# Optimization experiments

Measured on AMD Instinct MI355X. Metric: run time of the kernel, lower is better.

Reference implementation:

```python
import jax, jax.numpy as jnp
import numpy as np

EOS_IDX = 0  # CHARACTER_LIST.index(Config.EOS) stand-in


def _lstm_cell(x, h, c, W_ih, W_hh, b_ih, b_hh):
    # torch.nn.LSTMCell math; gate order i, f, g, o
    gates = x @ W_ih.T + b_ih + h @ W_hh.T + b_hh  # [B, 4H]
    i, f, g, o = jnp.split(gates, 4, axis=1)
    i = jax.nn.sigmoid(i)
    f = jax.nn.sigmoid(f)
    g = jnp.tanh(g)
    o = jax.nn.sigmoid(o)
    c_new = f * c + i * g
    h_new = o * jnp.tanh(c_new)
    return h_new, c_new


def setup_inputs() -> dict:
    key = jax.random.key(0)
    ks = jax.random.split(key, 13)
    B, T, V, E, H = 512, 256, 1000, 256, 512
    s = 0.05
    return {
        "listener_output": jax.random.normal(ks[0], (B, 128), jnp.float32),
        "ground_truth": jax.random.randint(ks[1], (B, T), 0, V, jnp.int64),
        "emb": jax.random.normal(ks[2], (V, E), jnp.float32) * s,
        "W_ih0": jax.random.normal(ks[3], (4 * H, E), jnp.float32) * s,
        "W_hh0": jax.random.normal(ks[4], (4 * H, H), jnp.float32) * s,
        "b_ih0": jax.random.normal(ks[5], (4 * H,), jnp.float32) * s,
        "b_hh0": jax.random.normal(ks[6], (4 * H,), jnp.float32) * s,
        "W_ih1": jax.random.normal(ks[7], (4 * H, E), jnp.float32) * s,
        "W_hh1": jax.random.normal(ks[8], (4 * H, H), jnp.float32) * s,
        "b_ih1": jax.random.normal(ks[9], (4 * H,), jnp.float32) * s,
        "b_hh1": jax.random.normal(ks[10], (4 * H,), jnp.float32) * s,
        "W_out": jax.random.normal(ks[11], (V, H), jnp.float32) * s,
        "b_out": jax.random.normal(ks[12], (V,), jnp.float32) * s,
    }


def reference(listener_output, ground_truth, emb, W_ih0, W_hh0, b_ih0, b_hh0,
              W_ih1, W_hh1, b_ih1, b_hh1, W_out, b_out):
    B = listener_output.shape[0]
    T = ground_truth.shape[1]
    H = W_hh0.shape[1]
    # Teacher forcing (ratio=1.0): input char at step 0 is EOS, then ground_truth[:, i-1]
    first = jnp.full((B, 1), EOS_IDX, dtype=ground_truth.dtype)
    chars = jnp.concatenate([first, ground_truth[:, :-1]], axis=1)  # [B, T]
    embeds = emb[chars]                                             # [B, T, E]
    xs = jnp.swapaxes(embeds, 0, 1)                                 # [T, B, E]

    h0 = jnp.zeros((B, H), embeds.dtype)
    c0 = jnp.zeros((B, H), embeds.dtype)
    h1 = jnp.zeros((B, H), embeds.dtype)
    c1 = jnp.zeros((B, H), embeds.dtype)

    def step(carry, x_t):
        h0, c0, h1, c1 = carry
        # Faithful to source: BOTH cells receive the embedding as input
        h0, c0 = _lstm_cell(x_t, h0, c0, W_ih0, W_hh0, b_ih0, b_hh0)
        h1, c1 = _lstm_cell(x_t, h1, c1, W_ih1, W_hh1, b_ih1, b_hh1)
        logits = h1 @ W_out.T + b_out                # [B, V]
        out = jax.nn.log_softmax(logits, axis=1)
        return (h0, c0, h1, c1), out

    _, outs = jax.lax.scan(step, (h0, c0, h1, c1), xs)  # [T, B, V]
    return jnp.swapaxes(outs, 0, 1)                     # [B, T, V]
```

## Files before the change

### kernel.cpp

```cpp
#include <hip/hip_runtime.h>
#include <hip/hip_bf16.h>

#define B_  512
#define T_  256
#define E_  256
#define H_  512
#define V_  1000
#define CH  16

typedef __attribute__((ext_vector_type(8))) short short8;
typedef __attribute__((ext_vector_type(4))) float f32x4;
typedef __hip_bfloat16 bf16;

#define MFMA16(a, b, c) __builtin_amdgcn_mfma_f32_16x16x32_bf16((a), (b), (c), 0, 0, 0)

__global__ void f32_to_bf16_kernel(const float* __restrict__ src,
                                   bf16* __restrict__ dst, int n8) {
  int i = blockIdx.x * blockDim.x + threadIdx.x;
  if (i >= n8) return;
  const float4* s4 = (const float4*)src;
  float4 a = s4[2 * i], b = s4[2 * i + 1];
  bf16 tmp[8] = {__float2bfloat16(a.x), __float2bfloat16(a.y),
                 __float2bfloat16(a.z), __float2bfloat16(a.w),
                 __float2bfloat16(b.x), __float2bfloat16(b.y),
                 __float2bfloat16(b.z), __float2bfloat16(b.w)};
  *(int4*)(dst + 8 * i) = *(const int4*)tmp;
}

__global__ __launch_bounds__(256) void embproj_kernel(
    const bf16* __restrict__ emb, const bf16* __restrict__ Wih,
    const float* __restrict__ b_ih, const float* __restrict__ b_hh,
    float* __restrict__ embProjB)
{
  __shared__ short As[64][40];
  __shared__ short Bs[64][40];
  const int tid  = threadIdx.x;
  const int wave = tid >> 6, lane = tid & 63;
  const int q = lane >> 4, col = lane & 15;
  const int m0 = blockIdx.x * 64;
  const int n0 = blockIdx.y * 64;
  const int sr  = tid >> 2, skc = (tid & 3) * 8;
  const int mr  = wave * 16 + col;
  const int ko  = q * 8;
  int arow = m0 + sr; if (arow > V_ - 1) arow = V_ - 1;

  f32x4 acc0 = {0.f,0.f,0.f,0.f}, acc1 = acc0, acc2 = acc0, acc3 = acc0;
  for (int k0 = 0; k0 < E_; k0 += 32) {
    *(int4*)&As[sr][skc] = *(const int4*)((const short*)emb + (size_t)arow * E_ + k0 + skc);
    *(int4*)&Bs[sr][skc] = *(const int4*)((const short*)Wih + (size_t)(n0 + sr) * E_ + k0 + skc);
    __syncthreads();
    short8 a  = *(const short8*)&As[mr][ko];
    short8 b0 = *(const short8*)&Bs[ 0 + col][ko];
    short8 b1 = *(const short8*)&Bs[16 + col][ko];
    short8 b2 = *(const short8*)&Bs[32 + col][ko];
    short8 b3 = *(const short8*)&Bs[48 + col][ko];
    acc0 = MFMA16(a, b0, acc0);
    acc1 = MFMA16(a, b1, acc1);
    acc2 = MFMA16(a, b2, acc2);
    acc3 = MFMA16(a, b3, acc3);
    __syncthreads();
  }
#pragma unroll
  for (int r = 0; r < 4; r++) {
    int m = m0 + wave * 16 + q * 4 + r;
    if (m < V_) {
      float* dst = embProjB + (size_t)m * 2048;
      int n = n0 + col;
      dst[n +  0] = acc0[r] + b_ih[n +  0] + b_hh[n +  0];
      dst[n + 16] = acc1[r] + b_ih[n + 16] + b_hh[n + 16];
      dst[n + 32] = acc2[r] + b_ih[n + 32] + b_hh[n + 32];
      dst[n + 48] = acc3[r] + b_ih[n + 48] + b_hh[n + 48];
    }
  }
}

__global__ __launch_bounds__(256) void recur_kernel(
    const int* __restrict__ gt,
    const bf16* __restrict__ Whh,
    const float* __restrict__ embProjB,
    const bf16* __restrict__ hprev0,
    bf16* __restrict__ h1buf,
    float* __restrict__ c_state,
    int* __restrict__ flags,
    int t0)
{
  __shared__ short Wl[64][520];
  __shared__ int chars[64];

  const int tid  = threadIdx.x;
  const int wave = tid >> 6, lane = tid & 63;
  const int q = lane >> 4, col = lane & 15;
  const int bid = blockIdx.x;
  const int mb = bid & 7, jb = bid >> 3;
  const int m0 = mb * 64, j0 = jb * 16;
  const int chunkv = (t0 >> 4) + 1;

  for (int cch = tid; cch < 64 * 64; cch += 256) {
    int r = cch >> 6, kc = (cch & 63) * 8;
    int gr = (r >> 4) * H_ + j0 + (r & 15);
    *(int4*)&Wl[r][kc] = *(const int4*)((const short*)Whh + (size_t)gr * H_ + kc);
  }

  const int mrow = m0 + wave * 16 + q * 4;
  const int arow = m0 + wave * 16 + col;

  float creg[4];
#pragma unroll
  for (int r = 0; r < 4; r++)
    creg[r] = c_state[(size_t)(mrow + r) * H_ + j0 + col];

  for (int s = 0; s < CH; s++) {
    const int t = t0 + s;
    if (tid < 64) chars[tid] = (t == 0) ? 0 : gt[(m0 + tid) * T_ + (t - 1)];
    if (s > 0 && tid < 32) {
      int* fl = flags + (((s - 1) * 8 + mb) << 5) + tid;
      while (__hip_atomic_load(fl, __ATOMIC_ACQUIRE, __HIP_MEMORY_SCOPE_AGENT) != chunkv) {}
    }
    __syncthreads();

    const bf16* hp = (s == 0) ? hprev0 : (h1buf + (size_t)(s - 1) * B_ * H_);

    float ex[4][4];
#pragma unroll
    for (int r = 0; r < 4; r++) {
      const float* ep = embProjB + (size_t)chars[wave * 16 + q * 4 + r] * 2048 + j0 + col;
#pragma unroll
      for (int g = 0; g < 4; g++) ex[g][r] = ep[g * H_];
    }

    f32x4 acc[4];
#pragma unroll
    for (int g = 0; g < 4; g++) acc[g] = (f32x4){0.f, 0.f, 0.f, 0.f};

    const short* abase = (const short*)hp + (size_t)arow * H_;
#pragma unroll
    for (int k0 = 0; k0 < H_; k0 += 32) {
      short8 a  = *(const short8*)(abase + k0 + q * 8);
      short8 b0 = *(const short8*)&Wl[ 0 + col][k0 + q * 8];
      short8 b1 = *(const short8*)&Wl[16 + col][k0 + q * 8];
      short8 b2 = *(const short8*)&Wl[32 + col][k0 + q * 8];
      short8 b3 = *(const short8*)&Wl[48 + col][k0 + q * 8];
      acc[0] = MFMA16(a, b0, acc[0]);
      acc[1] = MFMA16(a, b1, acc[1]);
      acc[2] = MFMA16(a, b2, acc[2]);
      acc[3] = MFMA16(a, b3, acc[3]);
    }

    bf16* ho = h1buf + (size_t)s * B_ * H_;
#pragma unroll
    for (int r = 0; r < 4; r++) {
      float iv = 1.f / (1.f + __expf(-(acc[0][r] + ex[0][r])));
      float fv = 1.f / (1.f + __expf(-(acc[1][r] + ex[1][r])));
      float gv = tanhf(acc[2][r] + ex[2][r]);
      float ov = 1.f / (1.f + __expf(-(acc[3][r] + ex[3][r])));
      float cN = fv * creg[r] + iv * gv;
      creg[r] = cN;
      ho[(size_t)(mrow + r) * H_ + j0 + col] = __float2bfloat16(ov * tanhf(cN));
    }

    __syncthreads();
    if (tid == 0)
      __hip_atomic_store(flags + ((s * 8 + mb) << 5) + jb, chunkv,
                         __ATOMIC_RELEASE, __HIP_MEMORY_SCOPE_AGENT);
  }

#pragma unroll
  for (int r = 0; r < 4; r++)
    c_state[(size_t)(mrow + r) * H_ + j0 + col] = creg[r];
}

__global__ __launch_bounds__(256) void out_proj_kernel(
    const bf16* __restrict__ h1buf,
    const bf16* __restrict__ Wout,
    const float* __restrict__ bout,
    float* __restrict__ out,
    int t0)
{
  __shared__ short Hs[32][520];
  __shared__ float red[4][32];
  __shared__ float rowM[32];
  __shared__ float rowS[32];

  const int tid  = threadIdx.x;
  const int wave = tid >> 6, lane = tid & 63;
  const int q = lane >> 4, col = lane & 15;
  const int s  = blockIdx.x >> 4;
  const int b0 = (blockIdx.x & 15) * 32;

  const short* hrow = (const short*)h1buf + ((size_t)s * B_ + b0) * H_;
  for (int c = tid; c < 2048; c += 256) {
    int r = c >> 6, kc = (c & 63) << 3;
    *(int4*)&Hs[r][kc] = *(const int4*)&hrow[r * H_ + kc];
  }
  __syncthreads();

  f32x4 acc[2][16];
#pragma unroll
  for (int mt = 0; mt < 2; mt++)
#pragma unroll
    for (int u = 0; u < 16; u++) acc[mt][u] = (f32x4){0.f, 0.f, 0.f, 0.f};

  const short* WS = (const short*)Wout;
  for (int k0 = 0; k0 < H_; k0 += 32) {
    short8 a0 = *(const short8*)&Hs[col][k0 + q * 8];
    short8 a1 = *(const short8*)&Hs[16 + col][k0 + q * 8];
#pragma unroll
    for (int u = 0; u < 16; u++) {
      int nt = wave + 4 * u;
      if (nt < 63) {
        int v = nt * 16 + col;
        int vc = v < V_ ? v : (V_ - 1);
        short8 bfr = *(const short8*)&WS[(size_t)vc * H_ + k0 + q * 8];
        acc[0][u] = MFMA16(a0, bfr, acc[0][u]);
        acc[1][u] = MFMA16(a1, bfr, acc[1][u]);
      }
    }
  }

  float bo[16];
  bool  val[16];
#pragma unroll
  for (int u = 0; u < 16; u++) {
    int nt = wave + 4 * u;
    int v = nt * 16 + col;
    val[u] = (nt < 63) && (v < V_);
    bo[u] = val[u] ? bout[v] : 0.f;
  }

  float mymax[2][4];
#pragma unroll
  for (int mt = 0; mt < 2; mt++)
#pragma unroll
    for (int r = 0; r < 4; r++) mymax[mt][r] = -1e30f;
#pragma unroll
  for (int mt = 0; mt < 2; mt++)
#pragma unroll
    for (int u = 0; u < 16; u++)
      if (val[u]) {
#pragma unroll
        for (int r = 0; r < 4; r++)
          mymax[mt][r] = fmaxf(mymax[mt][r], acc[mt][u][r] + bo[u]);
      }
#pragma unroll
  for (int d = 1; d < 16; d <<= 1)
#pragma unroll
    for (int mt = 0; mt < 2; mt++)
#pragma unroll
      for (int r = 0; r < 4; r++)
        mymax[mt][r] = fmaxf(mymax[mt][r], __shfl_xor(mymax[mt][r], d, 64));
  if (col == 0)
#pragma unroll
    for (int mt = 0; mt < 2; mt++)
#pragma unroll
      for (int r = 0; r < 4; r++)
        red[wave][mt * 16 + q * 4 + r] = mymax[mt][r];
  __syncthreads();
  if (tid < 32)
    rowM[tid] = fmaxf(fmaxf(red[0][tid], red[1][tid]),
                      fmaxf(red[2][tid], red[3][tid]));
  __syncthreads();

  float mysum[2][4] = {{0.f,0.f,0.f,0.f},{0.f,0.f,0.f,0.f}};
#pragma unroll
  for (int mt = 0; mt < 2; mt++)
#pragma unroll
    for (int r = 0; r < 4; r++) {
      float rm = rowM[mt * 16 + q * 4 + r];
#pragma unroll
      for (int u = 0; u < 16; u++)
        if (val[u]) mysum[mt][r] += __expf(acc[mt][u][r] + bo[u] - rm);
    }
#pragma unroll
  for (int d = 1; d < 16; d <<= 1)
#pragma unroll
    for (int mt = 0; mt < 2; mt++)
#pragma unroll
      for (int r = 0; r < 4; r++)
        mysum[mt][r] += __shfl_xor(mysum[mt][r], d, 64);
  if (col == 0)
#pragma unroll
    for (int mt = 0; mt < 2; mt++)
#pragma unroll
      for (int r = 0; r < 4; r++)
        red[wave][mt * 16 + q * 4 + r] = mysum[mt][r];
  __syncthreads();
  if (tid < 32)
    rowS[tid] = __logf(red[0][tid] + red[1][tid] + red[2][tid] + red[3][tid]);
  __syncthreads();

#pragma unroll
  for (int mt = 0; mt < 2; mt++)
#pragma unroll
    for (int r = 0; r < 4; r++) {
      int m = mt * 16 + q * 4 + r;
      float corr = rowM[m] + rowS[m];
      size_t base = ((size_t)(b0 + m) * T_ + (t0 + s)) * V_;
#pragma unroll
      for (int u = 0; u < 16; u++)
        if (val[u]) {
          int v = (wave + 4 * u) * 16 + col;
          out[base + v] = acc[mt][u][r] + bo[u] - corr;
        }
    }
}

extern "C" void kernel_launch(void* const* d_in, const int* in_sizes, int n_in,
                              void* d_out, int out_size, void* d_ws, size_t ws_size,
                              hipStream_t stream) {
  (void)in_sizes; (void)n_in; (void)out_size; (void)ws_size;
  const int*   gt     = (const int*)d_in[1];
  const float* emb_f  = (const float*)d_in[2];
  const float* Wih_f  = (const float*)d_in[7];
  const float* Whh_f  = (const float*)d_in[8];
  const float* b_ih1  = (const float*)d_in[9];
  const float* b_hh1  = (const float*)d_in[10];
  const float* Wout_f = (const float*)d_in[11];
  const float* bout   = (const float*)d_in[12];
  float* out = (float*)d_out;

  char* ws = (char*)d_ws;
  float* c_state = (float*)ws;
  bf16*  hinit   = (bf16*)(ws + 1048576);
  bf16*  h1buf   = (bf16*)(ws + 1572864);
  bf16*  emb_bf  = (bf16*)(ws + 9961472);
  bf16*  Wih_bf  = (bf16*)(ws + 10473472);
  bf16*  Whh_bf  = (bf16*)(ws + 11522048);
  bf16*  Wout_bf = (bf16*)(ws + 13619200);
  float* embP    = (float*)(ws + 14643200);
  int*   flags   = (int*)(ws + 22835200);

  hipMemsetAsync(d_ws, 0, 1572864, stream);
  hipMemsetAsync(flags, 0, 16384, stream);

  f32_to_bf16_kernel<<<(V_ * E_ / 8 + 255) / 256, 256, 0, stream>>>(emb_f, emb_bf, V_ * E_ / 8);
  f32_to_bf16_kernel<<<(4 * H_ * E_ / 8 + 255) / 256, 256, 0, stream>>>(Wih_f, Wih_bf, 4 * H_ * E_ / 8);
  f32_to_bf16_kernel<<<(4 * H_ * H_ / 8 + 255) / 256, 256, 0, stream>>>(Whh_f, Whh_bf, 4 * H_ * H_ / 8);
  f32_to_bf16_kernel<<<(V_ * H_ / 8 + 255) / 256, 256, 0, stream>>>(Wout_f, Wout_bf, V_ * H_ / 8);

  embproj_kernel<<<dim3(16, 32), 256, 0, stream>>>(emb_bf, Wih_bf, b_ih1, b_hh1, embP);

  for (int chunk = 0; chunk < T_ / CH; chunk++) {
    int t0 = chunk * CH;
    const bf16* hp0 = (chunk == 0) ? hinit : h1buf + (size_t)(CH - 1) * B_ * H_;
    recur_kernel<<<256, 256, 0, stream>>>(gt, Whh_bf, embP, hp0, h1buf, c_state,
                                          flags, t0);
    out_proj_kernel<<<16 * CH, 256, 0, stream>>>(h1buf, Wout_bf, bout, out, t0);
  }
}
```

Before: 3.879 ms.

## Use counter-based flags and preload chars to shorten per-step sync

Replaces the per-block flag array (32 flags polled by 32 threads) with a single atomic counter per step and row block. A single thread spins on it with relaxed loads and then issues an acquire fence. All ground-truth characters for the chunk are loaded into shared memory up front, and the embedding-projection loads are issued before the wait so they overlap the spin. The aim is to cut cross-block synchronization latency on the sequential critical path. Counters grow monotonically across chunks (target = 32*chunk), which relies on the flag memory being zeroed once at the start. The final step skips the increment.

```diff
diff --git a/kernel.cpp b/kernel.cpp
--- a/kernel.cpp
+++ b/kernel.cpp
@@ -85,7 +85,7 @@
     int t0)
 {
   __shared__ short Wl[64][520];
-  __shared__ int chars[64];
+  __shared__ int chars_l[CH][64];
 
   const int tid  = threadIdx.x;
   const int wave = tid >> 6, lane = tid & 63;
@@ -93,13 +93,19 @@
   const int bid = blockIdx.x;
   const int mb = bid & 7, jb = bid >> 3;
   const int m0 = mb * 64, j0 = jb * 16;
-  const int chunkv = (t0 >> 4) + 1;
+  const int target = 32 * ((t0 / CH) + 1);
 
   for (int cch = tid; cch < 64 * 64; cch += 256) {
     int r = cch >> 6, kc = (cch & 63) * 8;
     int gr = (r >> 4) * H_ + j0 + (r & 15);
     *(int4*)&Wl[r][kc] = *(const int4*)((const short*)Whh + (size_t)gr * H_ + kc);
   }
+  for (int idx = tid; idx < 64 * CH; idx += 256) {
+    int m = idx >> 4;
+    int s = idx & 15;
+    int t = t0 + s;
+    chars_l[s][m] = (t == 0) ? 0 : gt[(size_t)(m0 + m) * T_ + (t - 1)];
+  }
 
   const int mrow = m0 + wave * 16 + q * 4;
   const int arow = m0 + wave * 16 + col;
@@ -109,24 +115,29 @@
   for (int r = 0; r < 4; r++)
     creg[r] = c_state[(size_t)(mrow + r) * H_ + j0 + col];
 
+  __syncthreads();
+
   for (int s = 0; s < CH; s++) {
-    const int t = t0 + s;
-    if (tid < 64) chars[tid] = (t == 0) ? 0 : gt[(m0 + tid) * T_ + (t - 1)];
-    if (s > 0 && tid < 32) {
-      int* fl = flags + (((s - 1) * 8 + mb) << 5) + tid;
-      while (__hip_atomic_load(fl, __ATOMIC_ACQUIRE, __HIP_MEMORY_SCOPE_AGENT) != chunkv) {}
-    }
-    __syncthreads();
+    float ex[4][4];
+#pragma unroll
+    for (int r = 0; r < 4; r++) {
+      const float* ep =
+          embProjB + (size_t)chars_l[s][wave * 16 + q * 4 + r] * 2048 + j0 + col;
+#pragma unroll
+      for (int g = 0; g < 4; g++) ex[g][r] = ep[g * H_];
+    }
+
+    if (s > 0) {
+      if (tid == 0) {
+        int* fl = &flags[(s - 1) * 8 + mb];
+        while (__hip_atomic_load(fl, __ATOMIC_RELAXED,
+                                 __HIP_MEMORY_SCOPE_AGENT) < target) {}
+        __builtin_amdgcn_fence(__ATOMIC_ACQUIRE, "agent");
+      }
+      __syncthreads();
+    }
 
     const bf16* hp = (s == 0) ? hprev0 : (h1buf + (size_t)(s - 1) * B_ * H_);
-
-    float ex[4][4];
-#pragma unroll
-    for (int r = 0; r < 4; r++) {
-      const float* ep = embProjB + (size_t)chars[wave * 16 + q * 4 + r] * 2048 + j0 + col;
-#pragma unroll
-      for (int g = 0; g < 4; g++) ex[g][r] = ep[g * H_];
-    }
 
     f32x4 acc[4];
 #pragma unroll
@@ -159,9 +170,9 @@
     }
 
     __syncthreads();
-    if (tid == 0)
-      __hip_atomic_store(flags + ((s * 8 + mb) << 5) + jb, chunkv,
-                         __ATOMIC_RELEASE, __HIP_MEMORY_SCOPE_AGENT);
+    if (tid == 0 && s < CH - 1)
+      __hip_atomic_fetch_add(&flags[s * 8 + mb], 1, __ATOMIC_RELEASE,
+                             __HIP_MEMORY_SCOPE_AGENT);
   }
 
 #pragma unroll
@@ -330,7 +341,7 @@
   int*   flags   = (int*)(ws + 22835200);
 
   hipMemsetAsync(d_ws, 0, 1572864, stream);
-  hipMemsetAsync(flags, 0, 16384, stream);
+  hipMemsetAsync(flags, 0, 1024, stream);
 
   f32_to_bf16_kernel<<<(V_ * E_ / 8 + 255) / 256, 256, 0, stream>>>(emb_f, emb_bf, V_ * E_ / 8);
   f32_to_bf16_kernel<<<(4 * H_ * E_ / 8 + 255) / 256, 256, 0, stream>>>(Wih_f, Wih_bf, 4 * H_ * E_ / 8);
```

Result: slower. 4.652 ms (+19.9%).
